# Kernel optimization log

Measured on AMD Instinct MI355X. Metric: run time of the kernel, lower is better.

The kernel has to match this reference:

```python
import jax, jax.numpy as jnp
import numpy as np

N = 30000      # points
E = 400000     # edges
CIN = 16       # input point features
B = 4          # graphs in batch
H, W = 60, 80  # BEV grid


def _mlp_params(key, cin, cout):
    k1, k2 = jax.random.split(key)
    wa = jax.random.normal(k1, (cin, cout), jnp.float32) * np.float32(np.sqrt(2.0 / cin))
    wb = jax.random.normal(k2, (cout, cout), jnp.float32) * np.float32(np.sqrt(2.0 / cout))
    return wa, jnp.zeros((cout,), jnp.float32), wb, jnp.zeros((cout,), jnp.float32)


def setup_inputs() -> dict:
    key = jax.random.key(0)
    ks = jax.random.split(key, 8)
    x = jax.random.normal(ks[0], (N, CIN), jnp.float32)
    r = jax.random.uniform(ks[1], (N, 3), jnp.float32)
    Z = 1.0 + 9.0 * r[:, 2]
    X = (r[:, 0] - 0.5) * 1.2 * Z   # |X/Z| < 0.6 -> mostly inside image
    Y = (r[:, 1] - 0.5) * 0.9 * Z
    pos = jnp.stack([X, Y, Z], axis=1)
    edge_index = jax.random.randint(ks[2], (2, E), 0, N, jnp.int32)
    batch = jnp.sort(jax.random.randint(ks[3], (N,), 0, B, jnp.int32))
    K = jnp.array([[500.0, 0.0, 320.0], [0.0, 500.0, 240.0], [0.0, 0.0, 1.0]], jnp.float32)
    w11, b11, w12, b12 = _mlp_params(ks[4], CIN + 3, 64)
    w21, b21, w22, b22 = _mlp_params(ks[5], 64 + 3, 128)
    w31, b31, w32, b32 = _mlp_params(ks[6], 128 + 3, 256)
    return dict(x=x, pos=pos, K=K,
                w11=w11, b11=b11, w12=w12, b12=b12,
                w21=w21, b21=b21, w22=w22, b22=b22,
                w31=w31, b31=b31, w32=w32, b32=b32,
                edge_index=edge_index, batch=batch)


def _mlp(h, wa, ba, wb, bb):
    return jax.nn.relu(h @ wa + ba) @ wb + bb


def _pointnet_conv(feat, rel, src, dst, wa, ba, wb, bb):
    # PyG PointNetConv: msg = local_nn([x_j, pos_j - pos_i]); max-aggregate at target i
    msg = _mlp(jnp.concatenate([feat[src], rel], axis=1), wa, ba, wb, bb)
    agg = jax.ops.segment_max(msg, dst, num_segments=N)
    return jnp.where(jnp.isfinite(agg), agg, 0.0)  # empty segments -> 0 (PyG fill)


def _points_to_image(feat, pos, batch, K):
    X, Y, Z = pos[:, 0], pos[:, 1], pos[:, 2]
    u = ((K[0, 0] * X / Z + K[0, 2]) / 640.0 * W).astype(jnp.int32)  # trunc like .long()
    v = ((K[1, 1] * Y / Z + K[1, 2]) / 480.0 * H).astype(jnp.int32)
    mask = (u >= 0) & (u < W) & (v >= 0) & (v < H)
    idx = jnp.where(mask, batch * (H * W) + v * W + u, 0)
    contrib = feat * mask[:, None].astype(feat.dtype)
    flat = jnp.zeros((B * H * W, feat.shape[1]), feat.dtype).at[idx].add(contrib)
    return flat.reshape(B, H, W, feat.shape[1]).transpose(0, 3, 1, 2)


def reference(x, pos, K, w11, b11, w12, b12, w21, b21, w22, b22, w31, b31, w32, b32,
              edge_index, batch):
    src, dst = edge_index[0], edge_index[1]
    rel = pos[src] - pos[dst]
    h = _pointnet_conv(x, rel, src, dst, w11, b11, w12, b12)
    h = _pointnet_conv(h, rel, src, dst, w21, b21, w22, b22)
    h = _pointnet_conv(h, rel, src, dst, w31, b31, w32, b32)
    return _points_to_image(h, pos, batch, K)  # [B, 256, H, W]
```

## Files before the change

kernel.cpp:

```cpp
#include <hip/hip_runtime.h>
#include <math.h>

#define NN 30000
#define NE 400000

typedef _Float16 f16;
typedef _Float16 f16x8 __attribute__((ext_vector_type(8)));
typedef _Float16 f16x4 __attribute__((ext_vector_type(4)));
typedef float f32x4 __attribute__((ext_vector_type(4)));

__device__ __forceinline__ void atomic_max_f(float* addr, float v) {
    if (v >= 0.0f) {
        atomicMax((int*)addr, __float_as_int(v));
    } else {
        atomicMin((unsigned int*)addr, __float_as_uint(v));
    }
}

__global__ __launch_bounds__(256) void fill_neg_inf(float* p, int n) {
    int i = blockIdx.x * blockDim.x + threadIdx.x;
    int stride = gridDim.x * blockDim.x;
    for (; i < n; i += stride) p[i] = -INFINITY;
}

__global__ __launch_bounds__(256) void hist_dst(const int* __restrict__ dst,
                                                int* __restrict__ counts) {
    int e = blockIdx.x * 256 + threadIdx.x;
    if (e < NE) atomicAdd(&counts[dst[e]], 1);
}

__global__ __launch_bounds__(1024) void scan_counts(const int* __restrict__ counts,
                                                    int* __restrict__ cursor) {
    __shared__ int lsum[1024];
    const int t = threadIdx.x;
    const int base = t * 30;
    int s = 0;
    for (int i = 0; i < 30; ++i) {
        int idx = base + i;
        if (idx < NN) s += counts[idx];
    }
    lsum[t] = s;
    __syncthreads();
    int acc = s;
    for (int off = 1; off < 1024; off <<= 1) {
        int v = (t >= off) ? lsum[t - off] : 0;
        __syncthreads();
        acc += v;
        lsum[t] = acc;
        __syncthreads();
    }
    int run = acc - s;
    for (int i = 0; i < 30; ++i) {
        int idx = base + i;
        if (idx < NN) { cursor[idx] = run; run += counts[idx]; }
    }
}

__global__ __launch_bounds__(256) void scatter_edges(const int* __restrict__ src,
                                                     const int* __restrict__ dst,
                                                     int* __restrict__ cursor,
                                                     int* __restrict__ srcS,
                                                     int* __restrict__ dstS) {
    int e = blockIdx.x * 256 + threadIdx.x;
    if (e >= NE) return;
    int d = dst[e];
    int p = atomicAdd(&cursor[d], 1);
    srcS[p] = src[e];
    dstS[p] = d;
}

template<int K, int N>
__global__ __launch_bounds__(256) void pack_w(const float* __restrict__ wsrc,
                                              f16* __restrict__ pB) {
    int f = blockIdx.x * 256 + threadIdx.x;
    if (f >= K * N) return;
    int j = f & 7;
    int l = (f >> 3) & 63;
    int rest = f >> 9;
    constexpr int KS = K / 32;
    int ks = rest % KS;
    int nt = rest / KS;
    int k = ks * 32 + ((l >> 4) << 3) + j;
    int n = nt * 16 + (l & 15);
    pB[f] = (f16)wsrc[k * N + n];
}

__global__ __launch_bounds__(256) void cast_f16(const float* __restrict__ w,
                                                f16* __restrict__ o, int n) {
    int i = blockIdx.x * 256 + threadIdx.x;
    if (i < n) o[i] = (f16)w[i];
}

template<int K, int COUT>
__global__ __launch_bounds__(256) void node_linear(const float* __restrict__ feat,
                                                   const float* __restrict__ wa,
                                                   const float* __restrict__ b,
                                                   f16* __restrict__ A) {
    constexpr int NPB = 8;
    constexpr int G   = 256 / COUT;
    constexpr int NPT = NPB / G;
    __shared__ float sf[NPB * K];
    const int node0 = blockIdx.x * NPB;
    for (int idx = threadIdx.x; idx < NPB * K; idx += 256) {
        float v = feat[node0 * K + idx];
        if (!isfinite(v)) v = 0.0f;
        sf[idx] = v;
    }
    __syncthreads();
    const int j  = threadIdx.x % COUT;
    const int g  = threadIdx.x / COUT;
    const int n0 = g * NPT;
    float acc[NPT];
#pragma unroll
    for (int i = 0; i < NPT; i++) acc[i] = 0.0f;
    for (int k = 0; k < K; k++) {
        float w = wa[k * COUT + j];
#pragma unroll
        for (int nn = 0; nn < NPT; nn++)
            acc[nn] = fmaf(sf[(n0 + nn) * K + k], w, acc[nn]);
    }
    const float bj = b[j];
#pragma unroll
    for (int nn = 0; nn < NPT; nn++)
        A[(size_t)(node0 + n0 + nn) * COUT + j] = (f16)(acc[nn] + bj);
}

template<int K, int C>
__global__ __launch_bounds__(256) void node_gemm(const float* __restrict__ feat,
                                                 const f16* __restrict__ pW,
                                                 const float* __restrict__ bias,
                                                 f16* __restrict__ A) {
    constexpr int NTW = C / 64;
    constexpr int KS  = K / 32;
    __shared__ __align__(16) unsigned char smem[64 * K * 2];
    const int tid = threadIdx.x;
    const int node0 = blockIdx.x * 64;

    {
        const int e = tid >> 2, p = tid & 3;
        const bool valid = (node0 + e) < NN;
        const float* frow = feat + (size_t)(node0 + e) * K;
#pragma unroll
        for (int ch = 0; ch < K / 32; ++ch) {
            const int j0 = (ch * 4 + p) * 8;
            f16x8 hv;
#pragma unroll
            for (int jj = 0; jj < 8; ++jj) {
                float v = valid ? frow[j0 + jj] : 0.0f;
                if (!isfinite(v)) v = 0.0f;
                hv[jj] = (f16)v;
            }
            *(f16x8*)(smem + e * (K * 2) + ((j0 * 2) ^ ((e & 7) << 4))) = hv;
        }
    }
    __syncthreads();

    const int w = tid >> 6, l = tid & 63, lr = l & 15, lg = l >> 4;
    f32x4 acc[4][NTW] = {};
#pragma unroll
    for (int ks = 0; ks < KS; ++ks) {
        f16x8 af[4];
#pragma unroll
        for (int m = 0; m < 4; ++m) {
            const int row = m * 16 + lr;
            af[m] = *(const f16x8*)(smem + row * (K * 2)
                     + (((ks * 32 + lg * 8) * 2) ^ ((row & 7) << 4)));
        }
#pragma unroll
        for (int nt = 0; nt < NTW; ++nt) {
            const int ntg = w * NTW + nt;
            f16x8 bf = *(const f16x8*)(pW + ((size_t)(ntg * KS + ks) * 64 + l) * 8);
#pragma unroll
            for (int m = 0; m < 4; ++m)
                acc[m][nt] = __builtin_amdgcn_mfma_f32_16x16x32_f16(af[m], bf, acc[m][nt], 0, 0, 0);
        }
    }
#pragma unroll
    for (int m = 0; m < 4; ++m)
#pragma unroll
        for (int nt = 0; nt < NTW; ++nt) {
            const int col = w * (C / 4) + nt * 16 + lr;
            const float bv = bias[col];
#pragma unroll
            for (int rr = 0; rr < 4; ++rr) {
                const int row = m * 16 + lg * 4 + rr;
                if (node0 + row < NN)
                    A[(size_t)(node0 + row) * C + col] = (f16)(acc[m][nt][rr] + bv);
            }
        }
}

template<int C, int NW>
__global__ __launch_bounds__(NW * 64, 4) void edge_mfma(const f16* __restrict__ Ah,
                                                        const f16* __restrict__ warelh,
                                                        const f16* __restrict__ pB,
                                                        const float* __restrict__ bb,
                                                        const float* __restrict__ pos,
                                                        const int* __restrict__ srcS,
                                                        const int* __restrict__ dstS,
                                                        float* __restrict__ agg) {
    constexpr int TE   = 64;
    constexpr int BLK  = NW * 64;
    constexpr int CW   = C / NW;
    constexpr int NTW  = CW / 16;
    constexpr int KS   = C / 32;
    constexpr int CPR  = C / 8;
    constexpr int LOGC = (C == 256) ? 8 : (C == 128 ? 7 : 6);
    constexpr int LOGCPR = LOGC - 3;
    constexpr int SUB  = BLK / C;
    constexpr int SR   = 32 / SUB;
    static_assert(NTW >= 1 && SUB >= 1, "geometry");

    __shared__ __align__(16) unsigned char h1[TE * C * 2];
    __shared__ __align__(16) f16 s_warel[3 * C];
    __shared__ __align__(8)  f16 s_rel[TE][4];
    __shared__ int s_src[TE], s_dst[TE];

    const int tid = threadIdx.x;
    const int nwg = gridDim.x;
    const int q8 = nwg >> 3, r8 = nwg & 7;
    const int xcd = blockIdx.x & 7, o = blockIdx.x >> 3;
    const int bid = (xcd < r8 ? xcd * (q8 + 1) : r8 * (q8 + 1) + (xcd - r8) * q8) + o;
    const int e0 = bid * TE;

    if (tid < TE) {
        int s = srcS[e0 + tid], d = dstS[e0 + tid];
        s_src[tid] = s; s_dst[tid] = d;
        s_rel[tid][0] = (f16)(pos[3 * s + 0] - pos[3 * d + 0]);
        s_rel[tid][1] = (f16)(pos[3 * s + 1] - pos[3 * d + 1]);
        s_rel[tid][2] = (f16)(pos[3 * s + 2] - pos[3 * d + 2]);
        s_rel[tid][3] = (f16)0.f;
    }
    for (int i = tid; i < 3 * C / 8; i += BLK)
        ((f16x8*)s_warel)[i] = ((const f16x8*)warelh)[i];
    __syncthreads();

#pragma unroll
    for (int i = 0; i < (8 * C) / BLK; ++i) {
        const int g    = i * BLK + tid;
        const int row  = g >> LOGCPR;
        const int slot = g & (CPR - 1);
        const int s = s_src[row];
        const f16x4 rl = *(const f16x4*)&s_rel[row][0];
        const f16 rx = rl[0], ry = rl[1], rz = rl[2];
        const f16x8 rxv = {rx, rx, rx, rx, rx, rx, rx, rx};
        const f16x8 ryv = {ry, ry, ry, ry, ry, ry, ry, ry};
        const f16x8 rzv = {rz, rz, rz, rz, rz, rz, rz, rz};
        f16x8 av = *(const f16x8*)(Ah + (size_t)s * C + slot * 8);
        const f16* wp = s_warel + slot * 8;
        f16x8 w0 = *(const f16x8*)(wp);
        f16x8 w1 = *(const f16x8*)(wp + C);
        f16x8 w2 = *(const f16x8*)(wp + 2 * C);
        f16x8 hv = av + rxv * w0 + ryv * w1 + rzv * w2;
#pragma unroll
        for (int jj = 0; jj < 8; ++jj)
            hv[jj] = hv[jj] > (f16)0.f ? hv[jj] : (f16)0.f;
        *(f16x8*)(h1 + row * (2 * C) + ((slot * 16) ^ ((row & 7) << 4))) = hv;
    }
    __syncthreads();

    const int w = tid >> 6, l = tid & 63, lr = l & 15, lg = l >> 4;
    f32x4 acc[4][NTW] = {};
#pragma unroll
    for (int ks = 0; ks < KS; ++ks) {
        f16x8 af[4];
#pragma unroll
        for (int m = 0; m < 4; ++m) {
            const int row = m * 16 + lr;
            af[m] = *(const f16x8*)(h1 + row * (2 * C)
                     + (((ks * 32 + lg * 8) * 2) ^ ((row & 7) << 4)));
        }
#pragma unroll
        for (int nt = 0; nt < NTW; ++nt) {
            f16x8 bf = *(const f16x8*)(pB + ((size_t)((w * NTW + nt) * KS + ks) * 64 + l) * 8);
#pragma unroll
            for (int m = 0; m < 4; ++m)
                acc[m][nt] = __builtin_amdgcn_mfma_f32_16x16x32_f16(af[m], bf, acc[m][nt], 0, 0, 0);
        }
    }

    float* msg = (float*)h1;
    const int c  = tid & (C - 1);
    const int qq = tid >> LOGC;
    const float bbv = bb[c];
#pragma unroll
    for (int half = 0; half < 2; ++half) {
        __syncthreads();
#pragma unroll
        for (int mi = 0; mi < 2; ++mi) {
            const int m = half * 2 + mi;
#pragma unroll
            for (int nt = 0; nt < NTW; ++nt) {
                const int col = w * CW + nt * 16 + lr;
#pragma unroll
                for (int rr = 0; rr < 4; ++rr) {
                    const int row = m * 16 + lg * 4 + rr;
                    msg[(row - half * 32) * C + col] = acc[m][nt][rr];
                }
            }
        }
        __syncthreads();
        {
            const int r0 = qq * SR;
            int prev = s_dst[half * 32 + r0];
            float run = -INFINITY;
#pragma unroll
            for (int k = 0; k < SR; ++k) {
                const int r = r0 + k;
                const int d = s_dst[half * 32 + r];
                const float v = msg[r * C + c];
                if (d != prev) {
                    atomic_max_f(&agg[(size_t)prev * C + c], run + bbv);
                    run = v; prev = d;
                } else {
                    run = fmaxf(run, v);
                }
            }
            atomic_max_f(&agg[(size_t)prev * C + c], run + bbv);
        }
    }
}

__global__ __launch_bounds__(256) void scatter_img(const float* __restrict__ feat,
                                                   const float* __restrict__ pos,
                                                   const float* __restrict__ Km,
                                                   const int* __restrict__ batch,
                                                   float* __restrict__ img) {
    const int n = blockIdx.x;
    const float X = pos[3 * n + 0], Y = pos[3 * n + 1], Z = pos[3 * n + 2];
    const float k00 = Km[0], k02 = Km[2], k11 = Km[4], k12 = Km[5];
    const int u = (int)((k00 * X / Z + k02) / 640.0f * 80.0f);
    const int v = (int)((k11 * Y / Z + k12) / 480.0f * 60.0f);
    if (u < 0 || u >= 80 || v < 0 || v >= 60) return;
    const int p = (batch[n] * 60 + v) * 80 + u;
    const int c = threadIdx.x;
    float val = feat[(size_t)n * 256 + c];
    if (!isfinite(val)) val = 0.0f;
    atomicAdd(img + (size_t)p * 256 + c, val);
}

__global__ __launch_bounds__(256) void transpose_img(const float* __restrict__ img,
                                                     float* __restrict__ out) {
    __shared__ float tile[32][33];
    const int b = blockIdx.z;
    const int p0 = blockIdx.x * 32, c0 = blockIdx.y * 32;
    const float* src = img + (size_t)b * 4800 * 256;
    float* dst = out + (size_t)b * 256 * 4800;
    const int tx = threadIdx.x & 31, ty = threadIdx.x >> 5;
#pragma unroll
    for (int i = 0; i < 32; i += 8)
        tile[ty + i][tx] = src[(size_t)(p0 + ty + i) * 256 + c0 + tx];
    __syncthreads();
#pragma unroll
    for (int i = 0; i < 32; i += 8)
        dst[(size_t)(c0 + ty + i) * 4800 + p0 + tx] = tile[tx][ty + i];
}

extern "C" void kernel_launch(void* const* d_in, const int* in_sizes, int n_in,
                              void* d_out, int out_size, void* d_ws, size_t ws_size,
                              hipStream_t stream) {
    const float* x   = (const float*)d_in[0];
    const float* pos = (const float*)d_in[1];
    const float* Km  = (const float*)d_in[2];
    const float* w11 = (const float*)d_in[3];
    const float* b11 = (const float*)d_in[4];
    const float* w12 = (const float*)d_in[5];
    const float* b12 = (const float*)d_in[6];
    const float* w21 = (const float*)d_in[7];
    const float* b21 = (const float*)d_in[8];
    const float* w22 = (const float*)d_in[9];
    const float* b22 = (const float*)d_in[10];
    const float* w31 = (const float*)d_in[11];
    const float* b31 = (const float*)d_in[12];
    const float* w32 = (const float*)d_in[13];
    const float* b32 = (const float*)d_in[14];
    const int* edge  = (const int*)d_in[15];
    const int* batch = (const int*)d_in[16];
    const int* srcp = edge;
    const int* dstp = edge + NE;
    float* out = (float*)d_out;

    float* aggA  = (float*)d_ws;
    float* aggB  = aggA + (size_t)NN * 256;
    f16*   Ah    = (f16*)(aggB + (size_t)NN * 256);
    int*   srcS  = (int*)(Ah + (size_t)NN * 256);
    int*   dstS  = srcS + NE;
    int*   counts = dstS + NE;
    int*   cursor = counts + NN;
    f16*   pW1   = (f16*)(cursor + NN);
    f16*   pW2   = pW1 + 64 * 64;
    f16*   pW3   = pW2 + 128 * 128;
    f16*   pW2n  = pW3 + 256 * 256;
    f16*   pW3n  = pW2n + 64 * 128;
    f16*   wr1   = pW3n + 128 * 256;
    f16*   wr2   = wr1 + 3 * 64;
    f16*   wr3   = wr2 + 3 * 128;

    hipMemsetAsync(counts, 0, NN * sizeof(int), stream);
    hist_dst<<<(NE + 255) / 256, 256, 0, stream>>>(dstp, counts);
    scan_counts<<<1, 1024, 0, stream>>>(counts, cursor);
    scatter_edges<<<(NE + 255) / 256, 256, 0, stream>>>(srcp, dstp, cursor, srcS, dstS);

    pack_w<64, 64><<<(64 * 64 + 255) / 256, 256, 0, stream>>>(w12, pW1);
    pack_w<128, 128><<<(128 * 128 + 255) / 256, 256, 0, stream>>>(w22, pW2);
    pack_w<256, 256><<<(256 * 256 + 255) / 256, 256, 0, stream>>>(w32, pW3);
    pack_w<64, 128><<<(64 * 128 + 255) / 256, 256, 0, stream>>>(w21, pW2n);
    pack_w<128, 256><<<(128 * 256 + 255) / 256, 256, 0, stream>>>(w31, pW3n);
    cast_f16<<<1, 256, 0, stream>>>(w11 + 16 * 64, wr1, 3 * 64);
    cast_f16<<<2, 256, 0, stream>>>(w21 + 64 * 128, wr2, 3 * 128);
    cast_f16<<<3, 256, 0, stream>>>(w31 + 128 * 256, wr3, 3 * 256);

    node_linear<16, 64><<<NN / 8, 256, 0, stream>>>(x, w11, b11, Ah);
    fill_neg_inf<<<512, 256, 0, stream>>>(aggB, NN * 64);
    edge_mfma<64, 4><<<NE / 64, 256, 0, stream>>>(Ah, wr1, pW1, b12,
                                                  pos, srcS, dstS, aggB);
    node_gemm<64, 128><<<(NN + 63) / 64, 256, 0, stream>>>(aggB, pW2n, b21, Ah);
    fill_neg_inf<<<512, 256, 0, stream>>>(aggA, NN * 128);
    edge_mfma<128, 8><<<NE / 64, 512, 0, stream>>>(Ah, wr2, pW2, b22,
                                                   pos, srcS, dstS, aggA);
    node_gemm<128, 256><<<(NN + 63) / 64, 256, 0, stream>>>(aggA, pW3n, b31, Ah);
    fill_neg_inf<<<512, 256, 0, stream>>>(aggB, NN * 256);
    edge_mfma<256, 8><<<NE / 64, 512, 0, stream>>>(Ah, wr3, pW3, b32,
                                                   pos, srcS, dstS, aggB);
    hipMemsetAsync(aggA, 0, (size_t)4 * 4800 * 256 * sizeof(float), stream);
    scatter_img<<<NN, 256, 0, stream>>>(aggB, pos, Km, batch, aggA);
    transpose_img<<<dim3(150, 8, 4), 256, 0, stream>>>(aggA, out);
}
```

Measured before the change: 406.2 us.

## Reduce MFMA accumulators per destination segment in registers instead of via LDS

Replaces the epilogue that staged MFMA results to shared memory in two halves, with barriers, and then ran a serial segmented max per column. Segment boundaries in the sorted destination list are found with a wave ballot. For each segment, every lane takes the max over its accumulator rows in range, and cross-lane shuffles finish the reduction before one atomic max per column. This removes the LDS round trip and the __syncthreads calls. In exchange, the loop over segments is serial and wave-uniform, so tiles with many distinct destinations (random edges give close to 64 per tile) can execute many more iterations and shuffles.

New measurement: 382.5 us. 1.06x faster.

```diff
diff --git a/kernel.cpp b/kernel.cpp
--- a/kernel.cpp
+++ b/kernel.cpp
@@ -205,11 +205,8 @@
     constexpr int NTW  = CW / 16;
     constexpr int KS   = C / 32;
     constexpr int CPR  = C / 8;
-    constexpr int LOGC = (C == 256) ? 8 : (C == 128 ? 7 : 6);
-    constexpr int LOGCPR = LOGC - 3;
-    constexpr int SUB  = BLK / C;
-    constexpr int SR   = 32 / SUB;
-    static_assert(NTW >= 1 && SUB >= 1, "geometry");
+    constexpr int LOGCPR = (C == 256) ? 5 : (C == 128 ? 4 : 3);
+    static_assert(NTW >= 1, "geometry");
 
     __shared__ __align__(16) unsigned char h1[TE * C * 2];
     __shared__ __align__(16) f16 s_warel[3 * C];
@@ -279,44 +276,37 @@
         }
     }
 
-    float* msg = (float*)h1;
-    const int c  = tid & (C - 1);
-    const int qq = tid >> LOGC;
-    const float bbv = bb[c];
-#pragma unroll
-    for (int half = 0; half < 2; ++half) {
-        __syncthreads();
-#pragma unroll
-        for (int mi = 0; mi < 2; ++mi) {
-            const int m = half * 2 + mi;
-#pragma unroll
-            for (int nt = 0; nt < NTW; ++nt) {
-                const int col = w * CW + nt * 16 + lr;
+    float bbv[NTW];
+#pragma unroll
+    for (int nt = 0; nt < NTW; ++nt) bbv[nt] = bb[w * CW + nt * 16 + lr];
+
+    const int myd = s_dst[l];
+    const int pd  = s_dst[l == 0 ? 0 : l - 1];
+    unsigned long long m = __ballot((l == 0) || (myd != pd));
+
+    while (m) {
+        const int a = __builtin_ctzll(m);
+        const unsigned long long m2 = m & (m - 1);
+        const int b = m2 ? __builtin_ctzll(m2) : 64;
+        m = m2;
+        const int d = s_dst[a];
+#pragma unroll
+        for (int nt = 0; nt < NTW; ++nt) {
+            float v = -INFINITY;
+#pragma unroll
+            for (int mm = 0; mm < 4; ++mm) {
+                if (b <= mm * 16 || a >= mm * 16 + 16) continue;
 #pragma unroll
                 for (int rr = 0; rr < 4; ++rr) {
-                    const int row = m * 16 + lg * 4 + rr;
-                    msg[(row - half * 32) * C + col] = acc[m][nt][rr];
+                    const int row = mm * 16 + lg * 4 + rr;
+                    const bool in = (row >= a) && (row < b);
+                    v = fmaxf(v, in ? acc[mm][nt][rr] : -INFINITY);
                 }
             }
-        }
-        __syncthreads();
-        {
-            const int r0 = qq * SR;
-            int prev = s_dst[half * 32 + r0];
-            float run = -INFINITY;
-#pragma unroll
-            for (int k = 0; k < SR; ++k) {
-                const int r = r0 + k;
-                const int d = s_dst[half * 32 + r];
-                const float v = msg[r * C + c];
-                if (d != prev) {
-                    atomic_max_f(&agg[(size_t)prev * C + c], run + bbv);
-                    run = v; prev = d;
-                } else {
-                    run = fmaxf(run, v);
-                }
-            }
-            atomic_max_f(&agg[(size_t)prev * C + c], run + bbv);
+            v = fmaxf(v, __shfl_xor(v, 16, 64));
+            v = fmaxf(v, __shfl_xor(v, 32, 64));
+            if (lg == 0)
+                atomic_max_f(&agg[(size_t)d * C + w * CW + nt * 16 + lr], v + bbv[nt]);
         }
     }
 }
```
